# Performance work log

Hardware: AMD Instinct MI355X
Metric: run time of the kernel (lower is better)

The kernel has to match this reference:

```python
import jax, jax.numpy as jnp
import numpy as np

K = 64  # key_features
V = 64  # value_features


def setup_inputs() -> dict:
    key = jax.random.key(0)
    ks = jax.random.split(key, 7)
    B, IN, M = 512, 512, 2048
    H = 2 * K + V  # 192, hidden_state dim == output dim of layer
    return {
        "x": jax.random.normal(ks[0], (B, IN), dtype=jnp.float32),
        "hidden_state": jax.random.normal(ks[1], (B, H), dtype=jnp.float32),
        "content": jax.random.normal(ks[2], (B, V), dtype=jnp.float32),
        "key_mem": jax.random.normal(ks[3], (B, K, M), dtype=jnp.float32),
        "value_mem": jax.random.normal(ks[4], (B, V, M), dtype=jnp.float32),
        "W": jax.random.normal(ks[5], (H, IN + 2 * K + 2 * V), dtype=jnp.float32) * 0.02,
        "b": jax.random.normal(ks[6], (H,), dtype=jnp.float32) * 0.02,
    }


def reference(x, hidden_state, content, key_mem, value_mem, W, b):
    # dropout in eval mode (identity); relu on hidden_state
    inp = jnp.concatenate([x, jax.nn.relu(hidden_state), content], axis=1)  # [B, IN+2K+2V]
    o = inp @ W.T + b  # [B, 2K+V]
    query = o[:, :K]            # [B, K]
    # buffer.read: attention over memory slots
    scores = jnp.einsum("bkm,bk->bm", key_mem, query)   # [B, M]
    attn = jax.nn.softmax(scores, axis=1)               # [B, M]
    content_new = jnp.einsum("bvm,bm->bv", value_mem, attn)  # [B, V]
    # buffer.write (state update, returned for completeness of math; original
    # mutates buffer in place; key @ II is exactly a right-shift by one slot):
    new_key = o[:, K:2 * K]
    new_value = o[:, 2 * K:2 * K + V]
    key_mem_next = jnp.concatenate([new_key[:, :, None], key_mem[:, :, :-1]], axis=2)
    value_mem_next = jnp.concatenate([new_value[:, :, None], value_mem[:, :, :-1]], axis=2)
    del key_mem_next, value_mem_next  # forward output matches original: (o, content)
    return (o, content_new)
```

## Files before the change

### kernel.cpp

```cpp
#include <hip/hip_runtime.h>

#define KDIM 64
#define VDIM 64
#define MDIM 2048
#define BDIM 512
#define INDIM 512
#define HDIM 192
#define CIN 768
#define O_SIZE (BDIM*HDIM)

typedef float f32x4 __attribute__((ext_vector_type(4)));

__global__ __launch_bounds__(512, 4)
void memlinear_kernel(const float* __restrict__ x,
                      const float* __restrict__ hidden,
                      const float* __restrict__ content,
                      const float* __restrict__ key_mem,
                      const float* __restrict__ value_mem,
                      const float* __restrict__ W,
                      const float* __restrict__ bias,
                      float* __restrict__ out)
{
    const int b    = blockIdx.x;
    const int tid  = threadIdx.x;
    const int lane = tid & 63;
    const int wid  = tid >> 6;

    __shared__ __align__(16) float inp[CIN];
    __shared__ float q[KDIM];
    __shared__ float red[8];
    __shared__ __align__(16) float attn_lds[MDIM];

    if (tid < INDIM) inp[tid] = x[(size_t)b*INDIM + tid];
    if (tid < HDIM)  inp[INDIM + tid] = fmaxf(hidden[(size_t)b*HDIM + tid], 0.f);
    if (tid < VDIM)  inp[INDIM + HDIM + tid] = content[(size_t)b*VDIM + tid];
    __syncthreads();

    {
        const int j = tid >> 3;
        const int p = tid & 7;
        const float4* w4 = reinterpret_cast<const float4*>(W)
                           + (size_t)j * (CIN/4) + p * (CIN/32);
        const float4* i4 = reinterpret_cast<const float4*>(inp) + p * (CIN/32);
        float ax = 0.f, ay = 0.f, az = 0.f, aw = 0.f;
        #pragma unroll
        for (int r = 0; r < CIN/32; r += 8) {
            float4 wr[8];
            #pragma unroll
            for (int u = 0; u < 8; ++u) wr[u] = w4[r + u];
            #pragma unroll
            for (int u = 0; u < 8; ++u) {
                float4 v = i4[r + u];
                ax = fmaf(wr[u].x, v.x, ax);
                ay = fmaf(wr[u].y, v.y, ay);
                az = fmaf(wr[u].z, v.z, az);
                aw = fmaf(wr[u].w, v.w, aw);
            }
        }
        float pacc = (ax + ay) + (az + aw);
        pacc += __shfl_xor(pacc, 1);
        pacc += __shfl_xor(pacc, 2);
        pacc += __shfl_xor(pacc, 4);
        if (p == 0) {
            float o = pacc + bias[j];
            out[(size_t)b*HDIM + j] = o;
            q[j] = o;
        }
    }
    __syncthreads();

    const f32x4* km4 = reinterpret_cast<const f32x4*>(key_mem + (size_t)b*KDIM*MDIM);
    float sx = 0.f, sy = 0.f, sz = 0.f, sw = 0.f;
    #pragma unroll 8
    for (int k = 0; k < KDIM; ++k) {
        float qk = q[k];
        f32x4 kk = __builtin_nontemporal_load(km4 + (size_t)k*(MDIM/4) + tid);
        sx = fmaf(qk, kk.x, sx);
        sy = fmaf(qk, kk.y, sy);
        sz = fmaf(qk, kk.z, sz);
        sw = fmaf(qk, kk.w, sw);
    }

    float mx = fmaxf(fmaxf(sx, sy), fmaxf(sz, sw));
    #pragma unroll
    for (int off = 32; off >= 1; off >>= 1)
        mx = fmaxf(mx, __shfl_xor(mx, off));
    if (lane == 0) red[wid] = mx;
    __syncthreads();
    float m_all = red[0];
    #pragma unroll
    for (int w = 1; w < 8; ++w) m_all = fmaxf(m_all, red[w]);

    float ex = __expf(sx - m_all);
    float ey = __expf(sy - m_all);
    float ez = __expf(sz - m_all);
    float ew = __expf(sw - m_all);
    float sum = (ex + ey) + (ez + ew);
    #pragma unroll
    for (int off = 32; off >= 1; off >>= 1)
        sum += __shfl_xor(sum, off);
    __syncthreads();
    if (lane == 0) red[wid] = sum;
    __syncthreads();
    float total = 0.f;
    #pragma unroll
    for (int w = 0; w < 8; ++w) total += red[w];
    float inv = 1.0f / total;

    reinterpret_cast<float4*>(attn_lds)[tid] =
        make_float4(ex*inv, ey*inv, ez*inv, ew*inv);
    __syncthreads();

    const float4* vm4 = reinterpret_cast<const float4*>(value_mem + (size_t)b*VDIM*MDIM);
    const float4* a4  = reinterpret_cast<const float4*>(attn_lds);
    #pragma unroll
    for (int vi = 0; vi < 8; ++vi) {
        int v = wid*8 + vi;
        float px = 0.f, py = 0.f, pz = 0.f, pw = 0.f;
        #pragma unroll
        for (int i = 0; i < 8; ++i) {
            float4 vv = vm4[(size_t)v*(MDIM/4) + i*64 + lane];
            float4 aa = a4[i*64 + lane];
            px = fmaf(vv.x, aa.x, px);
            py = fmaf(vv.y, aa.y, py);
            pz = fmaf(vv.z, aa.z, pz);
            pw = fmaf(vv.w, aa.w, pw);
        }
        float p = (px + py) + (pz + pw);
        #pragma unroll
        for (int off = 32; off >= 1; off >>= 1)
            p += __shfl_xor(p, off);
        if (lane == 0) out[O_SIZE + (size_t)b*VDIM + v] = p;
    }

    {
        const int jj = tid >> 2;
        const int j  = KDIM + jj;
        const int p  = tid & 3;
        const float4* w4 = reinterpret_cast<const float4*>(W)
                           + (size_t)j * (CIN/4) + p * (CIN/16);
        const float4* i4 = reinterpret_cast<const float4*>(inp) + p * (CIN/16);
        float ax = 0.f, ay = 0.f, az = 0.f, aw = 0.f;
        #pragma unroll
        for (int r = 0; r < CIN/16; r += 8) {
            float4 wr[8];
            #pragma unroll
            for (int u = 0; u < 8; ++u) wr[u] = w4[r + u];
            #pragma unroll
            for (int u = 0; u < 8; ++u) {
                float4 v = i4[r + u];
                ax = fmaf(wr[u].x, v.x, ax);
                ay = fmaf(wr[u].y, v.y, ay);
                az = fmaf(wr[u].z, v.z, az);
                aw = fmaf(wr[u].w, v.w, aw);
            }
        }
        float pacc = (ax + ay) + (az + aw);
        pacc += __shfl_xor(pacc, 1);
        pacc += __shfl_xor(pacc, 2);
        if (p == 0) out[(size_t)b*HDIM + j] = pacc + bias[j];
    }
}

extern "C" void kernel_launch(void* const* d_in, const int* in_sizes, int n_in,
                              void* d_out, int out_size, void* d_ws, size_t ws_size,
                              hipStream_t stream) {
    const float* x         = (const float*)d_in[0];
    const float* hidden    = (const float*)d_in[1];
    const float* content   = (const float*)d_in[2];
    const float* key_mem   = (const float*)d_in[3];
    const float* value_mem = (const float*)d_in[4];
    const float* W         = (const float*)d_in[5];
    const float* bias      = (const float*)d_in[6];
    float* out = (float*)d_out;

    memlinear_kernel<<<dim3(BDIM), dim3(512), 0, stream>>>(
        x, hidden, content, key_mem, value_mem, W, bias, out);
}
```

Before: 116.2 us.

## Stream key_mem through a 4-deep LDS ring using async global_load_lds

The key-score loop now issues `__builtin_amdgcn_global_load_lds` copies straight into a 4-slot shared-memory ring, one key row per slot. Each step waits with an explicit `s_waitcnt vmcnt` and reads its float4 from LDS, replacing direct nontemporal global loads into registers. The goal is to keep several rows of key memory in flight without tying up vector registers, and to hide HBM latency with a software pipeline. The attention buffer now reuses ring slot 0. In exchange, LDS use grows, only four loads are in flight per thread, and correctness depends on hand-placed waitcnts and sched_barriers.

```diff
diff --git a/kernel.cpp b/kernel.cpp
--- a/kernel.cpp
+++ b/kernel.cpp
@@ -9,7 +9,8 @@
 #define CIN 768
 #define O_SIZE (BDIM*HDIM)
 
-typedef float f32x4 __attribute__((ext_vector_type(4)));
+typedef const float __attribute__((address_space(1))) gf32;
+typedef float __attribute__((address_space(3))) sf32;
 
 __global__ __launch_bounds__(512, 4)
 void memlinear_kernel(const float* __restrict__ x,
@@ -26,10 +27,10 @@
     const int lane = tid & 63;
     const int wid  = tid >> 6;
 
+    __shared__ __align__(16) float ring[4][MDIM];
     __shared__ __align__(16) float inp[CIN];
     __shared__ float q[KDIM];
     __shared__ float red[8];
-    __shared__ __align__(16) float attn_lds[MDIM];
 
     if (tid < INDIM) inp[tid] = x[(size_t)b*INDIM + tid];
     if (tid < HDIM)  inp[INDIM + tid] = fmaxf(hidden[(size_t)b*HDIM + tid], 0.f);
@@ -69,17 +70,38 @@
     }
     __syncthreads();
 
-    const f32x4* km4 = reinterpret_cast<const f32x4*>(key_mem + (size_t)b*KDIM*MDIM);
+    const float* krow = key_mem + (size_t)b*KDIM*MDIM + 4*tid;
+    #pragma unroll
+    for (int u = 0; u < 4; ++u)
+        __builtin_amdgcn_global_load_lds((gf32*)(krow + (size_t)u*MDIM),
+                                         (sf32*)&ring[u][wid*256], 16, 0, 2 );
     float sx = 0.f, sy = 0.f, sz = 0.f, sw = 0.f;
-    #pragma unroll 8
-    for (int k = 0; k < KDIM; ++k) {
-        float qk = q[k];
-        f32x4 kk = __builtin_nontemporal_load(km4 + (size_t)k*(MDIM/4) + tid);
-        sx = fmaf(qk, kk.x, sx);
-        sy = fmaf(qk, kk.y, sy);
-        sz = fmaf(qk, kk.z, sz);
-        sw = fmaf(qk, kk.w, sw);
-    }
+    #pragma unroll
+    for (int t = 0; t < KDIM - 4; ++t) {
+        asm volatile("s_waitcnt vmcnt(3)" ::: "memory");
+        __builtin_amdgcn_sched_barrier(0);
+        {
+            const float4 kk = *reinterpret_cast<const float4*>(
+                                  &ring[t & 3][wid*256 + 4*lane]);
+            const float qk = q[t];
+            sx = fmaf(qk, kk.x, sx); sy = fmaf(qk, kk.y, sy);
+            sz = fmaf(qk, kk.z, sz); sw = fmaf(qk, kk.w, sw);
+        }
+        __builtin_amdgcn_sched_barrier(0);
+        __builtin_amdgcn_global_load_lds((gf32*)(krow + (size_t)(t + 4)*MDIM),
+                                         (sf32*)&ring[t & 3][wid*256], 16, 0, 2);
+    }
+    #define KTAIL(t, n)                                                      \
+        asm volatile("s_waitcnt vmcnt(" #n ")" ::: "memory");                \
+        __builtin_amdgcn_sched_barrier(0);                                   \
+        {                                                                    \
+            const float4 kk = *reinterpret_cast<const float4*>(              \
+                                  &ring[(t) & 3][wid*256 + 4*lane]);         \
+            const float qk = q[t];                                           \
+            sx = fmaf(qk, kk.x, sx); sy = fmaf(qk, kk.y, sy);                \
+            sz = fmaf(qk, kk.z, sz); sw = fmaf(qk, kk.w, sw);                \
+        }
+    KTAIL(60, 3) KTAIL(61, 2) KTAIL(62, 1) KTAIL(63, 0)
 
     float mx = fmaxf(fmaxf(sx, sy), fmaxf(sz, sw));
     #pragma unroll
@@ -107,6 +129,7 @@
     for (int w = 0; w < 8; ++w) total += red[w];
     float inv = 1.0f / total;
 
+    float* attn_lds = ring[0];
     reinterpret_cast<float4*>(attn_lds)[tid] =
         make_float4(ex*inv, ey*inv, ez*inv, ew*inv);
     __syncthreads();
```

After: 117.7 us. No clear change (+1.3%).

## Split attention over memory halves per batch with flash-style combine kernel

Applied to the files above, without the earlier changes.

Each batch row's memory slots are split across two blocks, giving 1024 blocks instead of 512. Each block computes a partial softmax (max, sum, unnormalised weighted value sum) over its half and writes it to workspace, and a small second kernel merges the two halves with log-sum-exp rescaling. This is meant to raise parallelism across CUs for the memory-bound key/value streaming. In exchange the first linear layer's query rows are recomputed in both blocks, key loads become 8-byte instead of 16-byte, and an extra kernel launch is added.

```diff
diff --git a/kernel.cpp b/kernel.cpp
--- a/kernel.cpp
+++ b/kernel.cpp
@@ -8,20 +8,25 @@
 #define HDIM 192
 #define CIN 768
 #define O_SIZE (BDIM*HDIM)
-
-typedef float f32x4 __attribute__((ext_vector_type(4)));
+#define MH (MDIM/2)
+
+typedef float f32x2 __attribute__((ext_vector_type(2)));
 
 __global__ __launch_bounds__(512, 4)
-void memlinear_kernel(const float* __restrict__ x,
-                      const float* __restrict__ hidden,
-                      const float* __restrict__ content,
-                      const float* __restrict__ key_mem,
-                      const float* __restrict__ value_mem,
-                      const float* __restrict__ W,
-                      const float* __restrict__ bias,
-                      float* __restrict__ out)
+void attn_partial_kernel(const float* __restrict__ x,
+                         const float* __restrict__ hidden,
+                         const float* __restrict__ content,
+                         const float* __restrict__ key_mem,
+                         const float* __restrict__ value_mem,
+                         const float* __restrict__ W,
+                         const float* __restrict__ bias,
+                         float* __restrict__ out,
+                         float* __restrict__ wnum,
+                         float* __restrict__ wMS)
 {
-    const int b    = blockIdx.x;
+    const int bh   = blockIdx.x;
+    const int b    = bh >> 1;
+    const int h    = bh & 1;
     const int tid  = threadIdx.x;
     const int lane = tid & 63;
     const int wid  = tid >> 6;
@@ -29,7 +34,7 @@
     __shared__ __align__(16) float inp[CIN];
     __shared__ float q[KDIM];
     __shared__ float red[8];
-    __shared__ __align__(16) float attn_lds[MDIM];
+    __shared__ __align__(16) float attn_lds[MH];
 
     if (tid < INDIM) inp[tid] = x[(size_t)b*INDIM + tid];
     if (tid < HDIM)  inp[INDIM + tid] = fmaxf(hidden[(size_t)b*HDIM + tid], 0.f);
@@ -63,25 +68,24 @@
         pacc += __shfl_xor(pacc, 4);
         if (p == 0) {
             float o = pacc + bias[j];
-            out[(size_t)b*HDIM + j] = o;
+            if (h == 0) out[(size_t)b*HDIM + j] = o;
             q[j] = o;
         }
     }
     __syncthreads();
 
-    const f32x4* km4 = reinterpret_cast<const f32x4*>(key_mem + (size_t)b*KDIM*MDIM);
-    float sx = 0.f, sy = 0.f, sz = 0.f, sw = 0.f;
+    const f32x2* km2 = reinterpret_cast<const f32x2*>(
+                           key_mem + (size_t)b*KDIM*MDIM + h*MH) + tid;
+    float sx = 0.f, sy = 0.f;
     #pragma unroll 8
     for (int k = 0; k < KDIM; ++k) {
         float qk = q[k];
-        f32x4 kk = __builtin_nontemporal_load(km4 + (size_t)k*(MDIM/4) + tid);
+        f32x2 kk = __builtin_nontemporal_load(km2 + (size_t)k*(MDIM/2));
         sx = fmaf(qk, kk.x, sx);
         sy = fmaf(qk, kk.y, sy);
-        sz = fmaf(qk, kk.z, sz);
-        sw = fmaf(qk, kk.w, sw);
-    }
-
-    float mx = fmaxf(fmaxf(sx, sy), fmaxf(sz, sw));
+    }
+
+    float mx = fmaxf(sx, sy);
     #pragma unroll
     for (int off = 32; off >= 1; off >>= 1)
         mx = fmaxf(mx, __shfl_xor(mx, off));
@@ -93,9 +97,7 @@
 
     float ex = __expf(sx - m_all);
     float ey = __expf(sy - m_all);
-    float ez = __expf(sz - m_all);
-    float ew = __expf(sw - m_all);
-    float sum = (ex + ey) + (ez + ew);
+    float sum = ex + ey;
     #pragma unroll
     for (int off = 32; off >= 1; off >>= 1)
         sum += __shfl_xor(sum, off);
@@ -105,20 +107,23 @@
     float total = 0.f;
     #pragma unroll
     for (int w = 0; w < 8; ++w) total += red[w];
-    float inv = 1.0f / total;
-
-    reinterpret_cast<float4*>(attn_lds)[tid] =
-        make_float4(ex*inv, ey*inv, ez*inv, ew*inv);
-    __syncthreads();
-
-    const float4* vm4 = reinterpret_cast<const float4*>(value_mem + (size_t)b*VDIM*MDIM);
+
+    if (tid == 0) {
+        wMS[2*bh]     = m_all;
+        wMS[2*bh + 1] = total;
+    }
+    reinterpret_cast<float2*>(attn_lds)[tid] = make_float2(ex, ey);
+    __syncthreads();
+
+    const float4* vm4 = reinterpret_cast<const float4*>(
+                            value_mem + (size_t)b*VDIM*MDIM + h*MH);
     const float4* a4  = reinterpret_cast<const float4*>(attn_lds);
     #pragma unroll
     for (int vi = 0; vi < 8; ++vi) {
         int v = wid*8 + vi;
         float px = 0.f, py = 0.f, pz = 0.f, pw = 0.f;
         #pragma unroll
-        for (int i = 0; i < 8; ++i) {
+        for (int i = 0; i < 4; ++i) {
             float4 vv = vm4[(size_t)v*(MDIM/4) + i*64 + lane];
             float4 aa = a4[i*64 + lane];
             px = fmaf(vv.x, aa.x, px);
@@ -130,10 +135,10 @@
         #pragma unroll
         for (int off = 32; off >= 1; off >>= 1)
             p += __shfl_xor(p, off);
-        if (lane == 0) out[O_SIZE + (size_t)b*VDIM + v] = p;
-    }
-
-    {
+        if (lane == 0) wnum[(size_t)bh*VDIM + v] = p;
+    }
+
+    if (h == 0) {
         const int jj = tid >> 2;
         const int j  = KDIM + jj;
         const int p  = tid & 3;
@@ -160,6 +165,23 @@
         pacc += __shfl_xor(pacc, 2);
         if (p == 0) out[(size_t)b*HDIM + j] = pacc + bias[j];
     }
+}
+
+__global__ __launch_bounds__(64)
+void combine_kernel(const float* __restrict__ wnum,
+                    const float* __restrict__ wMS,
+                    float* __restrict__ out)
+{
+    const int b = blockIdx.x;
+    const int v = threadIdx.x;
+    const float M0 = wMS[4*b + 0], S0 = wMS[4*b + 1];
+    const float M1 = wMS[4*b + 2], S1 = wMS[4*b + 3];
+    const float M  = fmaxf(M0, M1);
+    const float a0 = __expf(M0 - M), a1 = __expf(M1 - M);
+    const float den = S0*a0 + S1*a1;
+    const float num = wnum[(size_t)(2*b)*VDIM + v]*a0
+                    + wnum[(size_t)(2*b + 1)*VDIM + v]*a1;
+    out[O_SIZE + (size_t)b*VDIM + v] = num / den;
 }
 
 extern "C" void kernel_launch(void* const* d_in, const int* in_sizes, int n_in,
@@ -172,8 +194,11 @@
     const float* value_mem = (const float*)d_in[4];
     const float* W         = (const float*)d_in[5];
     const float* bias      = (const float*)d_in[6];
-    float* out = (float*)d_out;
-
-    memlinear_kernel<<<dim3(BDIM), dim3(512), 0, stream>>>(
-        x, hidden, content, key_mem, value_mem, W, bias, out);
+    float* out  = (float*)d_out;
+    float* wnum = (float*)d_ws;
+    float* wMS  = wnum + 1024*VDIM;
+
+    attn_partial_kernel<<<dim3(2*BDIM), dim3(512), 0, stream>>>(
+        x, hidden, content, key_mem, value_mem, W, bias, out, wnum, wMS);
+    combine_kernel<<<dim3(BDIM), dim3(64), 0, stream>>>(wnum, wMS, out);
 }
```

Result: slower. 158.8 us (+36.6%).
